# Kernel tuning notes

Measured on AMD Instinct MI355X. Metric: run time of the kernel, lower is better.

The kernel has to match this reference:

```python
import jax, jax.numpy as jnp
import numpy as np


def _conv1x1(x, w, b=None):
    # x: (N,C,H,W), w: (O,C) -> (N,O,H,W)
    y = jnp.einsum('nchw,oc->nohw', x, w)
    return y if b is None else y + b[None, :, None, None]


def _norm(f):
    # per-channel zero-mean / unit-std over (N,H,W); torch.std is unbiased (ddof=1)
    mean = f.mean(axis=(0, 2, 3), keepdims=True)
    std = f.std(axis=(0, 2, 3), ddof=1, keepdims=True)
    return (f - mean) / (std + 1e-6)


def _causal_attention(x, w_cls):
    N, C, H, W = x.shape
    M = _conv1x1(x, w_cls).reshape(N, -1, H * W)     # (N,K,HW)
    sm = jax.nn.softmax(M, axis=2)                   # softmax over spatial
    return jnp.einsum('nkp,ncp->nkc', sm, x.reshape(N, C, H * W))  # (N,K,C)


def _ccnet(x, wq, bq, wk, bk, wv, bv, gamma1):
    B, C, H, W = x.shape
    q = _conv1x1(x, wq, bq)  # (B,Cq,H,W)
    k = _conv1x1(x, wk, bk)
    v = _conv1x1(x, wv, bv)  # (B,C,H,W)
    # column (vertical) attention energies with -inf on the self diagonal
    eH = jnp.einsum('bciw,bcjw->biwj', q, k)         # (B,H,W,H)
    eH = jnp.where(jnp.eye(H, dtype=bool)[None, :, None, :], -jnp.inf, eH)
    # row (horizontal) attention energies
    eW = jnp.einsum('bchi,bchj->bhij', q, k)         # (B,H,W,W)
    att = jax.nn.softmax(jnp.concatenate([eH, eW], axis=3), axis=3)
    attH, attW = att[..., :H], att[..., H:]
    outH = jnp.einsum('bcjw,biwj->bciw', v, attH)    # aggregate along column
    outW = jnp.einsum('bchj,bhij->bchi', v, attW)    # aggregate along row
    return gamma1 * (outH + outW) + x


def setup_inputs() -> dict:
    key = jax.random.key(0)
    ks = jax.random.split(key, 10)
    B, C, H, W = 8, 256, 96, 96
    Cq, K = C // 8, 6
    f32 = jnp.float32
    return {
        'preds_S': jax.random.normal(ks[0], (B, C, H, W), f32),
        'preds_T': jax.random.normal(ks[1], (B, C, H, W), f32),
        'w_cls': jax.random.normal(ks[2], (K, C), f32) * 0.05,
        'wq': jax.random.normal(ks[3], (Cq, C), f32) * 0.05,
        'bq': jnp.zeros((Cq,), f32),
        'wk': jax.random.normal(ks[4], (Cq, C), f32) * 0.05,
        'bk': jnp.zeros((Cq,), f32),
        'wv': jax.random.normal(ks[5], (C, C), f32) * 0.05,
        'bv': jnp.zeros((C,), f32),
        'gamma1': jax.random.normal(ks[6], (1,), f32) * 0.1,
    }


def reference(preds_S, preds_T, w_cls, wq, bq, wk, bk, wv, bv, gamma1):
    CA_W, CC_W = 0.0005, 1e-05
    N = preds_S.shape[0]
    s = _norm(preds_S)
    t = _norm(preds_T)
    ca_t = _causal_attention(t, w_cls)
    ca_s = _causal_attention(s, w_cls)
    ca_loss = jnp.sum((ca_t - ca_s) ** 2) / N
    cc_t = _ccnet(t, wq, bq, wk, bk, wv, bv, gamma1)
    cc_s = _ccnet(s, wq, bq, wk, bk, wv, bv, gamma1)
    cc_loss = jnp.sum((cc_t - cc_s) ** 2) / N
    return ca_loss * CA_W + cc_loss * CC_W
```

## Files before the change

kernel.cpp:

```cpp
#include <hip/hip_runtime.h>
#include <math.h>

#define NBAT 8
#define NC   256
#define NH   96
#define NW   96
#define NP   9216
#define NCQ  32
#define NKC  6
#define NL   192
#define NV   320
#define NTOT 73728

typedef __attribute__((ext_vector_type(4))) float  floatx4;
typedef __attribute__((ext_vector_type(8))) short  short8;

__device__ __forceinline__ float bf2f(unsigned short h){
  return __uint_as_float(((unsigned)h) << 16);
}
__device__ __forceinline__ float bflo(unsigned u){ return __uint_as_float(u << 16); }
__device__ __forceinline__ float bfhi(unsigned u){ return __uint_as_float(u & 0xFFFF0000u); }
__device__ __forceinline__ unsigned short f2bf(float f){
  unsigned u = __float_as_uint(f);
  u += 0x7FFFu + ((u >> 16) & 1u);
  return (unsigned short)(u >> 16);
}

union F4 { float4 v; float a[4]; };

__device__ __forceinline__ float warpReduceSum(float v){
  #pragma unroll
  for (int m = 32; m; m >>= 1) v += __shfl_xor(v, m);
  return v;
}
__device__ __forceinline__ float warpReduceMax(float v){
  #pragma unroll
  for (int m = 32; m; m >>= 1) v = fmaxf(v, __shfl_xor(v, m));
  return v;
}
__device__ float blockReduceSum(float v){
  __shared__ float lds[8];
  v = warpReduceSum(v);
  int wid = threadIdx.x >> 6, lane = threadIdx.x & 63;
  int nw = blockDim.x >> 6;
  if (lane == 0) lds[wid] = v;
  __syncthreads();
  if (wid == 0){
    v = (lane < nw) ? lds[lane] : 0.f;
    #pragma unroll
    for (int m = 4; m; m >>= 1) v += __shfl_xor(v, m);
  }
  __syncthreads();
  return v;
}
__device__ float blockReduceMax(float v){
  __shared__ float lds[8];
  v = warpReduceMax(v);
  int wid = threadIdx.x >> 6, lane = threadIdx.x & 63;
  int nw = blockDim.x >> 6;
  if (lane == 0) lds[wid] = v;
  __syncthreads();
  if (wid == 0){
    v = (lane < nw) ? lds[lane] : -INFINITY;
    #pragma unroll
    for (int m = 4; m; m >>= 1) v = fmaxf(v, __shfl_xor(v, m));
  }
  __syncthreads();
  return v;
}

__global__ __launch_bounds__(256)
void k_stats(const float* __restrict__ S, const float* __restrict__ T,
             float* __restrict__ s_sum, float* __restrict__ s_sq){
  int blk = blockIdx.x;
  int t = blk / (NC * NBAT);
  int rem = blk % (NC * NBAT);
  int c = rem / NBAT;
  int n = rem % NBAT;
  const float4* x4 = (const float4*)((t ? T : S) + ((size_t)n * NC + c) * NP);
  float s = 0.f, q = 0.f;
  for (int p = threadIdx.x; p < NP / 4; p += 256){
    F4 f; f.v = x4[p];
    #pragma unroll
    for (int j = 0; j < 4; j++){ s += f.a[j]; q += f.a[j] * f.a[j]; }
  }
  s = blockReduceSum(s);
  q = blockReduceSum(q);
  if (threadIdx.x == 0){
    atomicAdd(&s_sum[t * NC + c], s);
    atomicAdd(&s_sq[t * NC + c], q);
  }
}

__global__ __launch_bounds__(512)
void k_finalize(const float* __restrict__ s_sum, const float* __restrict__ s_sq,
                float* __restrict__ mean, float* __restrict__ inv){
  int i = threadIdx.x;
  if (i < 2 * NC){
    float s = s_sum[i], q = s_sq[i];
    float m = s / (float)NTOT;
    float var = (q - s * m) / (float)(NTOT - 1);
    var = fmaxf(var, 0.f);
    mean[i] = m;
    inv[i] = 1.f / (sqrtf(var) + 1e-6f);
  }
}

__global__ __launch_bounds__(256)
void k_caM(const float* __restrict__ S, const float* __restrict__ T,
           const float* __restrict__ wcls,
           const float* __restrict__ mean, const float* __restrict__ inv,
           float* __restrict__ smca){
  int pt = blockIdx.x, n = blockIdx.y, t = blockIdx.z;
  __shared__ float wsc[NKC * NC];
  __shared__ float shift[NKC];
  for (int idx = threadIdx.x; idx < NKC * NC; idx += 256){
    int c = idx & 255;
    wsc[idx] = wcls[idx] * inv[t * NC + c];
  }
  __syncthreads();
  if (threadIdx.x < NKC){
    float sh = 0.f;
    for (int c = 0; c < NC; c++) sh += wsc[threadIdx.x * NC + c] * mean[t * NC + c];
    shift[threadIdx.x] = sh;
  }
  __syncthreads();
  int p = pt * 256 + threadIdx.x;
  const float* x = (t ? T : S) + (size_t)n * NC * NP + p;
  float acc[NKC];
  #pragma unroll
  for (int k = 0; k < NKC; k++) acc[k] = 0.f;
  for (int c = 0; c < NC; c++){
    float xv = x[(size_t)c * NP];
    #pragma unroll
    for (int k = 0; k < NKC; k++) acc[k] += wsc[k * NC + c] * xv;
  }
  size_t base = ((size_t)(t * NBAT + n) * NKC) * NP + p;
  #pragma unroll
  for (int k = 0; k < NKC; k++) smca[base + (size_t)k * NP] = acc[k] - shift[k];
}

__global__ __launch_bounds__(256)
void k_caSoftmax(float* __restrict__ smca){
  int r = blockIdx.x;
  float* row = smca + (size_t)r * NP;
  float m = -INFINITY;
  for (int p = threadIdx.x; p < NP; p += 256) m = fmaxf(m, row[p]);
  m = blockReduceMax(m);
  __shared__ float bm, bs;
  if (threadIdx.x == 0) bm = m;
  __syncthreads();
  m = bm;
  float s = 0.f;
  for (int p = threadIdx.x; p < NP; p += 256) s += expf(row[p] - m);
  s = blockReduceSum(s);
  if (threadIdx.x == 0) bs = 1.f / s;
  __syncthreads();
  float rs = bs;
  for (int p = threadIdx.x; p < NP; p += 256) row[p] = expf(row[p] - m) * rs;
}

__global__ __launch_bounds__(256)
void k_caOut(const float* __restrict__ S, const float* __restrict__ T,
             const float* __restrict__ smca,
             const float* __restrict__ mean, const float* __restrict__ inv,
             float* __restrict__ ca){
  int ct = blockIdx.x & 7, ks = blockIdx.x >> 3;
  int n = blockIdx.y, t = blockIdx.z;
  int c0 = ct * 32;
  __shared__ float xt[32 * 264];
  __shared__ float smt[NKC * 256];
  int cl = threadIdx.x >> 3, pl = threadIdx.x & 7;
  float acc[NKC];
  #pragma unroll
  for (int k = 0; k < NKC; k++) acc[k] = 0.f;
  const float* xbase = (t ? T : S) + (size_t)n * NC * NP;
  const float* smbase = smca + (size_t)(t * NBAT + n) * NKC * NP;
  for (int pt = ks * 6; pt < ks * 6 + 6; pt++){
    int p0 = pt * 256;
    for (int idx = threadIdx.x; idx < 32 * 256; idx += 256){
      int r = idx >> 8, p = idx & 255;
      float v = xbase[(size_t)(c0 + r) * NP + p0 + p];
      xt[r * 264 + p] = (v - mean[t * NC + c0 + r]) * inv[t * NC + c0 + r];
    }
    for (int idx = threadIdx.x; idx < NKC * 256; idx += 256){
      int k = idx >> 8, p = idx & 255;
      smt[idx] = smbase[(size_t)k * NP + p0 + p];
    }
    __syncthreads();
    for (int j = 0; j < 32; j++){
      float xv = xt[cl * 264 + pl + 8 * j];
      #pragma unroll
      for (int k = 0; k < NKC; k++) acc[k] += smt[k * 256 + pl + 8 * j] * xv;
    }
    __syncthreads();
  }
  #pragma unroll
  for (int k = 0; k < NKC; k++){
    float v = acc[k];
    v += __shfl_xor(v, 1); v += __shfl_xor(v, 2); v += __shfl_xor(v, 4);
    if (pl == 0) atomicAdd(&ca[((size_t)(t * NBAT + n) * NKC + k) * NC + c0 + cl], v);
  }
}

__global__ __launch_bounds__(256)
void k_caLoss(const float* __restrict__ ca, float* __restrict__ out){
  int i = blockIdx.x * 256 + threadIdx.x;
  float d = 0.f;
  if (i < NBAT * NKC * NC) d = ca[(size_t)NBAT * NKC * NC + i] - ca[i];
  float ss = blockReduceSum(d * d);
  if (threadIdx.x == 0) atomicAdd(out, ss * (0.0005f / 8.0f));
}

__global__ __launch_bounds__(256)
void k_xn(const float* __restrict__ x0, int b0,
          const float* __restrict__ mean, const float* __restrict__ inv, int t,
          unsigned short* __restrict__ XN){
  int pt = blockIdx.x, ct = blockIdx.y, bb = blockIdx.z;
  int bg = b0 + bb;
  int p0 = pt * 64, c0 = ct * 64;
  __shared__ float tile[64 * 65];
  const float* x = x0 + ((size_t)bg * NC + c0) * NP + p0;
  #pragma unroll
  for (int i = 0; i < 4; i++){
    int idx = threadIdx.x + i * 256;
    int r = idx >> 4, g = (idx & 15) * 4;
    F4 f; f.v = *(const float4*)(x + (size_t)r * NP + g);
    float m = mean[t * NC + c0 + r], iv = inv[t * NC + c0 + r];
    #pragma unroll
    for (int j = 0; j < 4; j++) tile[(g + j) * 65 + r] = (f.a[j] - m) * iv;
  }
  __syncthreads();
  #pragma unroll
  for (int i = 0; i < 4; i++){
    int idx = threadIdx.x + i * 256;
    int p = idx >> 4, g = (idx & 15) * 4;
    unsigned lo = (unsigned)f2bf(tile[p * 65 + g + 0]) | ((unsigned)f2bf(tile[p * 65 + g + 1]) << 16);
    unsigned hi = (unsigned)f2bf(tile[p * 65 + g + 2]) | ((unsigned)f2bf(tile[p * 65 + g + 3]) << 16);
    uint2 u; u.x = lo; u.y = hi;
    *(uint2*)(XN + ((size_t)bb * NP + p0 + p) * NC + c0 + g) = u;
  }
}

__global__ __launch_bounds__(256)
void k_wconv(const float* __restrict__ wv, const float* __restrict__ wq,
             const float* __restrict__ wk, unsigned short* __restrict__ Wb){
  int n = blockIdx.x;
  const float* src = (n < 256) ? (wv + (size_t)n * NC)
                   : (n < 288) ? (wq + (size_t)(n - 256) * NC)
                               : (wk + (size_t)(n - 288) * NC);
  Wb[(size_t)n * NC + threadIdx.x] = f2bf(src[threadIdx.x]);
}

__global__ __launch_bounds__(256)
void k_v(const unsigned short* __restrict__ XN, const unsigned short* __restrict__ Wb,
         const float* __restrict__ bv, const float* __restrict__ bq,
         const float* __restrict__ bk,
         unsigned short* __restrict__ VT1,
         unsigned short* __restrict__ qb, unsigned short* __restrict__ kb){
  int pt = blockIdx.x, bb = blockIdx.y;
  int p0 = pt * 64;
  __shared__ unsigned short Wl[NV * 40];
  int lane = threadIdx.x & 63;
  int wid = threadIdx.x >> 6;
  int col = lane & 15, quad = lane >> 4;
  const unsigned short* xnb = XN + (size_t)bb * NP * NC + (size_t)(p0 + wid * 16 + col) * NC;
  floatx4 acc[20];
  #pragma unroll
  for (int nt = 0; nt < 20; nt++) acc[nt] = (floatx4){0.f, 0.f, 0.f, 0.f};

  int ci_n[5], ci_k8[5];
  #pragma unroll
  for (int i = 0; i < 5; i++){ int ci = i * 256 + threadIdx.x; ci_n[i] = ci >> 2; ci_k8[i] = (ci & 3) * 8; }

  short8 w[5];
  #pragma unroll
  for (int i = 0; i < 5; i++)
    w[i] = *(const short8*)(Wb + (size_t)ci_n[i] * NC + ci_k8[i]);

  for (int ks = 0; ks < 8; ks++){
    if (ks) __syncthreads();
    #pragma unroll
    for (int i = 0; i < 5; i++)
      *(short8*)(Wl + ci_n[i] * 40 + ci_k8[i]) = w[i];
    __syncthreads();
    if (ks < 7){
      int k0n = (ks + 1) * 32;
      #pragma unroll
      for (int i = 0; i < 5; i++)
        w[i] = *(const short8*)(Wb + (size_t)ci_n[i] * NC + k0n + ci_k8[i]);
    }
    short8 a = *(const short8*)(xnb + ks * 32 + quad * 8);
    #pragma unroll
    for (int nt = 0; nt < 20; nt++){
      short8 b = *(const short8*)(Wl + (nt * 16 + col) * 40 + quad * 8);
      acc[nt] = __builtin_amdgcn_mfma_f32_16x16x32_bf16(a, b, acc[nt], 0, 0, 0);
    }
  }

  int prow0 = p0 + wid * 16 + quad * 4;
  #pragma unroll
  for (int nt = 0; nt < 16; nt++){
    int c = nt * 16 + col;
    float bias = bv[c];
    uint2 u;
    u.x = (unsigned)f2bf(acc[nt][0] + bias) | ((unsigned)f2bf(acc[nt][1] + bias) << 16);
    u.y = (unsigned)f2bf(acc[nt][2] + bias) | ((unsigned)f2bf(acc[nt][3] + bias) << 16);
    *(uint2*)(VT1 + ((size_t)bb * NC + c) * NP + prow0) = u;
  }
  #pragma unroll
  for (int nt = 16; nt < 18; nt++){
    int c = (nt - 16) * 16 + col;
    float bias = bq[c];
    #pragma unroll
    for (int i = 0; i < 4; i++)
      qb[((size_t)bb * NP + prow0 + i) * NCQ + c] = f2bf(acc[nt][i] + bias);
  }
  #pragma unroll
  for (int nt = 18; nt < 20; nt++){
    int c = (nt - 18) * 16 + col;
    float bias = bk[c];
    #pragma unroll
    for (int i = 0; i < 4; i++)
      kb[((size_t)bb * NP + prow0 + i) * NCQ + c] = f2bf(acc[nt][i] + bias);
  }
}

__global__ __launch_bounds__(256)
void k_vt(const unsigned short* __restrict__ VT1, unsigned short* __restrict__ VT2){
  int c = blockIdx.x, bb = blockIdx.y;
  __shared__ unsigned short tile[96 * 104];
  size_t base = ((size_t)bb * NC + c) * NP;
  for (int idx = threadIdx.x; idx < 1152; idx += 256){
    int h = idx / 12, g = idx % 12;
    short8 v = *(const short8*)(VT1 + base + h * 96 + g * 8);
    #pragma unroll
    for (int kk = 0; kk < 8; kk++) tile[(g * 8 + kk) * 104 + h] = ((unsigned short*)&v)[kk];
  }
  __syncthreads();
  for (int idx = threadIdx.x; idx < 1152; idx += 256){
    int w = idx / 12, g = idx % 12;
    short8 v = *(const short8*)(tile + w * 104 + g * 8);
    *(short8*)(VT2 + base + w * 96 + g * 8) = v;
  }
}

__global__ __launch_bounds__(256)
void k_e(const unsigned short* __restrict__ qb, const unsigned short* __restrict__ kb,
         unsigned short* __restrict__ att){
  int x = blockIdx.x, bb = blockIdx.y, which = blockIdx.z;
  int lane = threadIdx.x & 63, wid = threadIdx.x >> 6;
  int col = lane & 15, quad = lane >> 4;
  int mi0 = (wid & 1) * 3, ni0 = (wid >> 1) * 3;
  short8 a[3], b[3];
  if (which == 0){
    #pragma unroll
    for (int m = 0; m < 3; m++)
      a[m] = *(const short8*)(qb + ((size_t)bb * NP + ((mi0 + m) * 16 + col) * 96 + x) * NCQ + quad * 8);
    #pragma unroll
    for (int n = 0; n < 3; n++)
      b[n] = *(const short8*)(kb + ((size_t)bb * NP + ((ni0 + n) * 16 + col) * 96 + x) * NCQ + quad * 8);
  } else {
    #pragma unroll
    for (int m = 0; m < 3; m++)
      a[m] = *(const short8*)(qb + ((size_t)bb * NP + x * 96 + (mi0 + m) * 16 + col) * NCQ + quad * 8);
    #pragma unroll
    for (int n = 0; n < 3; n++)
      b[n] = *(const short8*)(kb + ((size_t)bb * NP + x * 96 + (ni0 + n) * 16 + col) * NCQ + quad * 8);
  }
  floatx4 acc[3][3];
  #pragma unroll
  for (int m = 0; m < 3; m++)
    #pragma unroll
    for (int n = 0; n < 3; n++){
      acc[m][n] = (floatx4){0.f, 0.f, 0.f, 0.f};
      acc[m][n] = __builtin_amdgcn_mfma_f32_16x16x32_bf16(a[m], b[n], acc[m][n], 0, 0, 0);
    }
  #pragma unroll
  for (int m = 0; m < 3; m++)
    #pragma unroll
    for (int n = 0; n < 3; n++){
      int j = (ni0 + n) * 16 + col;
      #pragma unroll
      for (int r = 0; r < 4; r++){
        int i = (mi0 + m) * 16 + quad * 4 + r;
        int p = which ? (x * 96 + i) : (i * 96 + x);
        float v = (!which && j == i) ? -INFINITY : acc[m][n][r];
        att[((size_t)bb * NP + p) * NL + (which ? 96 + j : j)] = f2bf(v);
      }
    }
}

__global__ __launch_bounds__(256)
void k_attSoftmax(unsigned short* __restrict__ att){
  int q = blockIdx.x * 4 + (threadIdx.x >> 6);
  int lane = threadIdx.x & 63;
  unsigned short* row = att + (size_t)q * NL;
  float e0 = bf2f(row[lane]);
  float e1 = bf2f(row[64 + lane]);
  float e2 = bf2f(row[128 + lane]);
  float m = fmaxf(e0, fmaxf(e1, e2));
  m = warpReduceMax(m);
  float x0 = expf(e0 - m), x1 = expf(e1 - m), x2 = expf(e2 - m);
  float s = warpReduceSum(x0 + x1 + x2);
  float rs = 1.f / s;
  row[lane]       = f2bf(x0 * rs);
  row[64 + lane]  = f2bf(x1 * rs);
  row[128 + lane] = f2bf(x2 * rs);
}

__global__ __launch_bounds__(256)
void k_outH(const unsigned short* __restrict__ VT2, const unsigned short* __restrict__ att,
            unsigned short* __restrict__ OH){
  int w = blockIdx.x, bb = blockIdx.y, cs = blockIdx.z;
  int lane = threadIdx.x & 63, wid = threadIdx.x >> 6;
  int col = lane & 15, quad = lane >> 4;
  int c = cs * 64 + wid * 16 + col;
  floatx4 acc[6];
  #pragma unroll
  for (int m = 0; m < 6; m++) acc[m] = (floatx4){0.f, 0.f, 0.f, 0.f};
  #pragma unroll
  for (int ks = 0; ks < 3; ks++){
    int k0 = ks * 32 + quad * 8;
    short8 a[6], b;
    #pragma unroll
    for (int m = 0; m < 6; m++)
      a[m] = *(const short8*)(att + ((size_t)bb * NP + (m * 16 + col) * 96 + w) * NL + k0);
    b = *(const short8*)(VT2 + ((size_t)bb * NC + c) * NP + w * 96 + k0);
    #pragma unroll
    for (int m = 0; m < 6; m++)
      acc[m] = __builtin_amdgcn_mfma_f32_16x16x32_bf16(a[m], b, acc[m], 0, 0, 0);
  }
  #pragma unroll
  for (int m = 0; m < 6; m++){
    #pragma unroll
    for (int r = 0; r < 4; r++){
      int i = m * 16 + quad * 4 + r;
      OH[((size_t)bb * NP + i * 96 + w) * NC + c] = f2bf(acc[m][r]);
    }
  }
}

__global__ __launch_bounds__(256)
void k_outW(const unsigned short* __restrict__ VT1, const unsigned short* __restrict__ att,
            const unsigned short* __restrict__ OH, unsigned short* __restrict__ Ot,
            const float* __restrict__ predsS, const float* __restrict__ predsT,
            const float* __restrict__ mean, const float* __restrict__ inv,
            const float* __restrict__ gamma, int b0, int spass,
            float* __restrict__ out){
  int h = blockIdx.x, bb = blockIdx.y, cs = blockIdx.z;
  int lane = threadIdx.x & 63, wid = threadIdx.x >> 6;
  int col = lane & 15, quad = lane >> 4;
  int c = cs * 64 + wid * 16 + col;
  floatx4 acc[6];
  #pragma unroll
  for (int m = 0; m < 6; m++) acc[m] = (floatx4){0.f, 0.f, 0.f, 0.f};
  #pragma unroll
  for (int ks = 0; ks < 3; ks++){
    int k0 = ks * 32 + quad * 8;
    short8 a[6], b;
    #pragma unroll
    for (int m = 0; m < 6; m++)
      a[m] = *(const short8*)(att + ((size_t)bb * NP + h * 96 + m * 16 + col) * NL + 96 + k0);
    b = *(const short8*)(VT1 + ((size_t)bb * NC + c) * NP + h * 96 + k0);
    #pragma unroll
    for (int m = 0; m < 6; m++)
      acc[m] = __builtin_amdgcn_mfma_f32_16x16x32_bf16(a[m], b, acc[m], 0, 0, 0);
  }
  if (!spass){
    #pragma unroll
    for (int m = 0; m < 6; m++){
      #pragma unroll
      for (int r = 0; r < 4; r++){
        int i = m * 16 + quad * 4 + r;
        size_t base = ((size_t)bb * NP + h * 96 + i) * NC + c;
        Ot[base] = f2bf(acc[m][r] + bf2f(OH[base]));
      }
    }
  } else {
    int bg = b0 + bb;
    float g = gamma[0];
    float ss = 0.f;
    float mS = mean[c],      iS = inv[c];
    float mT = mean[NC + c], iT = inv[NC + c];
    const float* tp = predsT + ((size_t)bg * NC + c) * NP + h * 96;
    const float* sp = predsS + ((size_t)bg * NC + c) * NP + h * 96;
    #pragma unroll
    for (int m = 0; m < 6; m++){
      int i0 = m * 16 + quad * 4;
      F4 tv, sv;
      tv.v = *(const float4*)(tp + i0);
      sv.v = *(const float4*)(sp + i0);
      #pragma unroll
      for (int r = 0; r < 4; r++){
        size_t base = ((size_t)bb * NP + h * 96 + i0 + r) * NC + c;
        float os = acc[m][r] + bf2f(OH[base]);
        float ot = bf2f(Ot[base]);
        float dn = (tv.a[r] - mT) * iT - (sv.a[r] - mS) * iS;
        float d = g * (ot - os) + dn;
        ss += d * d;
      }
    }
    ss = blockReduceSum(ss);
    if (threadIdx.x == 0) atomicAdd(out, ss * (1e-5f / 8.0f));
  }
}

extern "C" void kernel_launch(void* const* d_in, const int* in_sizes, int n_in,
                              void* d_out, int out_size, void* d_ws, size_t ws_size,
                              hipStream_t stream){
  (void)in_sizes; (void)n_in; (void)out_size;
  const float* S    = (const float*)d_in[0];
  const float* T    = (const float*)d_in[1];
  const float* wcls = (const float*)d_in[2];
  const float* wq   = (const float*)d_in[3];
  const float* bq   = (const float*)d_in[4];
  const float* wk   = (const float*)d_in[5];
  const float* bk   = (const float*)d_in[6];
  const float* wv   = (const float*)d_in[7];
  const float* bv   = (const float*)d_in[8];
  const float* gamma= (const float*)d_in[9];
  float* out = (float*)d_out;

  char* base = (char*)d_ws;
  size_t off = 0;
  auto alloc = [&](size_t b){ size_t o = off; off += (b + 255) & ~(size_t)255; return o; };
  size_t o_ssum = alloc(2 * NC * 4);
  size_t o_ssq  = alloc(2 * NC * 4);
  size_t o_mean = alloc(2 * NC * 4);
  size_t o_inv  = alloc(2 * NC * 4);
  size_t o_wb   = alloc((size_t)NV * NC * 2);
  size_t o_ca   = alloc((size_t)2 * NBAT * NKC * NC * 4);
  size_t o_smca = alloc((size_t)2 * NBAT * NKC * NP * 4);
  size_t fixed = off;
  size_t per_b = (size_t)NP * NC * 2 * 4
               + (size_t)NP * NCQ * 2 * 2
               + (size_t)NP * NL * 2;
  int NB = 8;
  while (NB > 1 && fixed + (size_t)NB * per_b + 8192 > ws_size) NB >>= 1;

  size_t o_xn  = alloc((size_t)NB * NP * NC * 2);
  size_t o_v1  = alloc((size_t)NB * NP * NC * 2);
  size_t o_v2  = alloc((size_t)NB * NP * NC * 2);
  size_t o_q   = alloc((size_t)NB * NP * NCQ * 2);
  size_t o_k   = alloc((size_t)NB * NP * NCQ * 2);
  size_t o_att = alloc((size_t)NB * NP * NL * 2);
  size_t o_ot  = alloc((size_t)NB * NP * NC * 2);
  size_t o_oh  = o_xn;

  float* ssum = (float*)(base + o_ssum);
  float* ssq  = (float*)(base + o_ssq);
  float* mean = (float*)(base + o_mean);
  float* inv  = (float*)(base + o_inv);
  float* ca   = (float*)(base + o_ca);
  float* smca = (float*)(base + o_smca);
  unsigned short* Wb  = (unsigned short*)(base + o_wb);
  unsigned short* XN  = (unsigned short*)(base + o_xn);
  unsigned short* VT1 = (unsigned short*)(base + o_v1);
  unsigned short* VT2 = (unsigned short*)(base + o_v2);
  unsigned short* qbp = (unsigned short*)(base + o_q);
  unsigned short* kbp = (unsigned short*)(base + o_k);
  unsigned short* att = (unsigned short*)(base + o_att);
  unsigned short* OH  = (unsigned short*)(base + o_oh);
  unsigned short* Ot  = (unsigned short*)(base + o_ot);

  hipMemsetAsync(d_out, 0, 4, stream);
  hipMemsetAsync(base + o_ssum, 0, 4096, stream);
  hipMemsetAsync(base + o_ca, 0, (size_t)2 * NBAT * NKC * NC * 4, stream);

  k_stats<<<dim3(2 * NC * NBAT), 256, 0, stream>>>(S, T, ssum, ssq);
  k_finalize<<<1, 512, 0, stream>>>(ssum, ssq, mean, inv);
  k_wconv<<<dim3(NV), 256, 0, stream>>>(wv, wq, wk, Wb);

  k_caM<<<dim3(36, NBAT, 2), 256, 0, stream>>>(S, T, wcls, mean, inv, smca);
  k_caSoftmax<<<dim3(2 * NBAT * NKC), 256, 0, stream>>>(smca);
  k_caOut<<<dim3(48, NBAT, 2), 256, 0, stream>>>(S, T, smca, mean, inv, ca);
  k_caLoss<<<dim3(48), 256, 0, stream>>>(ca, out);

  for (int b0 = 0; b0 < NBAT; b0 += NB){
    for (int pass = 0; pass < 2; pass++){
      int t = (pass == 0) ? 1 : 0;
      const float* x = t ? T : S;
      k_xn<<<dim3(144, 4, NB), 256, 0, stream>>>(x, b0, mean, inv, t, XN);
      k_v<<<dim3(144, NB), 256, 0, stream>>>(XN, Wb, bv, bq, bk, VT1, qbp, kbp);
      k_vt<<<dim3(NC, NB), 256, 0, stream>>>(VT1, VT2);
      k_e<<<dim3(96, NB, 2), 256, 0, stream>>>(qbp, kbp, att);
      k_attSoftmax<<<dim3(NB * 2304), 256, 0, stream>>>(att);
      k_outH<<<dim3(96, NB, 4), 256, 0, stream>>>(VT2, att, OH);
      k_outW<<<dim3(96, NB, 4), 256, 0, stream>>>(VT1, att, OH, Ot, S, T, mean, inv,
                                                  gamma, b0, pass, out);
    }
  }
}
```

Baseline: 689.2 us.

## Process teacher and student per batch together and fuse output-W with loss

The CCNet section now loops over one batch at a time and handles the teacher and student streams in the same launches, using a grid dimension to select between them. This replaces the earlier two passes over a multi-batch chunk. The new k_outWL kernel computes both outW results, stages both outH tiles in shared memory, and reduces the loss directly, so the intermediate Ot buffer is no longer written and read back. The smaller per-batch working set may stay resident in cache. In exchange there are many more, smaller kernel launches whose grids may not fill the GPU.

```diff
diff --git a/kernel.cpp b/kernel.cpp
--- a/kernel.cpp
+++ b/kernel.cpp
@@ -18,8 +18,6 @@
 __device__ __forceinline__ float bf2f(unsigned short h){
   return __uint_as_float(((unsigned)h) << 16);
 }
-__device__ __forceinline__ float bflo(unsigned u){ return __uint_as_float(u << 16); }
-__device__ __forceinline__ float bfhi(unsigned u){ return __uint_as_float(u & 0xFFFF0000u); }
 __device__ __forceinline__ unsigned short f2bf(float f){
   unsigned u = __float_as_uint(f);
   u += 0x7FFFu + ((u >> 16) & 1u);
@@ -213,11 +211,13 @@
 }
 
 __global__ __launch_bounds__(256)
-void k_xn(const float* __restrict__ x0, int b0,
-          const float* __restrict__ mean, const float* __restrict__ inv, int t,
-          unsigned short* __restrict__ XN){
-  int pt = blockIdx.x, ct = blockIdx.y, bb = blockIdx.z;
-  int bg = b0 + bb;
+void k_xn(const float* __restrict__ S, const float* __restrict__ T, int bg,
+          const float* __restrict__ mean, const float* __restrict__ inv,
+          unsigned short* __restrict__ XNT, unsigned short* __restrict__ XNS){
+  int pt = blockIdx.x, ct = blockIdx.y, ts = blockIdx.z;
+  int t = ts ? 0 : 1;
+  const float* x0 = ts ? S : T;
+  unsigned short* XN = ts ? XNS : XNT;
   int p0 = pt * 64, c0 = ct * 64;
   __shared__ float tile[64 * 65];
   const float* x = x0 + ((size_t)bg * NC + c0) * NP + p0;
@@ -238,7 +238,7 @@
     unsigned lo = (unsigned)f2bf(tile[p * 65 + g + 0]) | ((unsigned)f2bf(tile[p * 65 + g + 1]) << 16);
     unsigned hi = (unsigned)f2bf(tile[p * 65 + g + 2]) | ((unsigned)f2bf(tile[p * 65 + g + 3]) << 16);
     uint2 u; u.x = lo; u.y = hi;
-    *(uint2*)(XN + ((size_t)bb * NP + p0 + p) * NC + c0 + g) = u;
+    *(uint2*)(XN + ((size_t)(p0 + p)) * NC + c0 + g) = u;
   }
 }
 
@@ -253,18 +253,24 @@
 }
 
 __global__ __launch_bounds__(256)
-void k_v(const unsigned short* __restrict__ XN, const unsigned short* __restrict__ Wb,
+void k_v(const unsigned short* __restrict__ XNT, const unsigned short* __restrict__ XNS,
+         const unsigned short* __restrict__ Wb,
          const float* __restrict__ bv, const float* __restrict__ bq,
          const float* __restrict__ bk,
-         unsigned short* __restrict__ VT1,
-         unsigned short* __restrict__ qb, unsigned short* __restrict__ kb){
-  int pt = blockIdx.x, bb = blockIdx.y;
+         unsigned short* __restrict__ VT1T, unsigned short* __restrict__ VT1S,
+         unsigned short* __restrict__ qT, unsigned short* __restrict__ kT,
+         unsigned short* __restrict__ qS, unsigned short* __restrict__ kS){
+  int pt = blockIdx.x, ts = blockIdx.y;
+  const unsigned short* XN = ts ? XNS : XNT;
+  unsigned short* VT1 = ts ? VT1S : VT1T;
+  unsigned short* qb  = ts ? qS : qT;
+  unsigned short* kb  = ts ? kS : kT;
   int p0 = pt * 64;
   __shared__ unsigned short Wl[NV * 40];
   int lane = threadIdx.x & 63;
   int wid = threadIdx.x >> 6;
   int col = lane & 15, quad = lane >> 4;
-  const unsigned short* xnb = XN + (size_t)bb * NP * NC + (size_t)(p0 + wid * 16 + col) * NC;
+  const unsigned short* xnb = XN + (size_t)(p0 + wid * 16 + col) * NC;
   floatx4 acc[20];
   #pragma unroll
   for (int nt = 0; nt < 20; nt++) acc[nt] = (floatx4){0.f, 0.f, 0.f, 0.f};
@@ -306,7 +312,7 @@
     uint2 u;
     u.x = (unsigned)f2bf(acc[nt][0] + bias) | ((unsigned)f2bf(acc[nt][1] + bias) << 16);
     u.y = (unsigned)f2bf(acc[nt][2] + bias) | ((unsigned)f2bf(acc[nt][3] + bias) << 16);
-    *(uint2*)(VT1 + ((size_t)bb * NC + c) * NP + prow0) = u;
+    *(uint2*)(VT1 + (size_t)c * NP + prow0) = u;
   }
   #pragma unroll
   for (int nt = 16; nt < 18; nt++){
@@ -314,7 +320,7 @@
     float bias = bq[c];
     #pragma unroll
     for (int i = 0; i < 4; i++)
-      qb[((size_t)bb * NP + prow0 + i) * NCQ + c] = f2bf(acc[nt][i] + bias);
+      qb[((size_t)(prow0 + i)) * NCQ + c] = f2bf(acc[nt][i] + bias);
   }
   #pragma unroll
   for (int nt = 18; nt < 20; nt++){
@@ -322,15 +328,18 @@
     float bias = bk[c];
     #pragma unroll
     for (int i = 0; i < 4; i++)
-      kb[((size_t)bb * NP + prow0 + i) * NCQ + c] = f2bf(acc[nt][i] + bias);
-  }
-}
-
-__global__ __launch_bounds__(256)
-void k_vt(const unsigned short* __restrict__ VT1, unsigned short* __restrict__ VT2){
-  int c = blockIdx.x, bb = blockIdx.y;
+      kb[((size_t)(prow0 + i)) * NCQ + c] = f2bf(acc[nt][i] + bias);
+  }
+}
+
+__global__ __launch_bounds__(256)
+void k_vt(const unsigned short* __restrict__ VT1T, const unsigned short* __restrict__ VT1S,
+          unsigned short* __restrict__ VT2T, unsigned short* __restrict__ VT2S){
+  int c = blockIdx.x, ts = blockIdx.y;
+  const unsigned short* VT1 = ts ? VT1S : VT1T;
+  unsigned short* VT2 = ts ? VT2S : VT2T;
   __shared__ unsigned short tile[96 * 104];
-  size_t base = ((size_t)bb * NC + c) * NP;
+  size_t base = (size_t)c * NP;
   for (int idx = threadIdx.x; idx < 1152; idx += 256){
     int h = idx / 12, g = idx % 12;
     short8 v = *(const short8*)(VT1 + base + h * 96 + g * 8);
@@ -346,9 +355,13 @@
 }
 
 __global__ __launch_bounds__(256)
-void k_e(const unsigned short* __restrict__ qb, const unsigned short* __restrict__ kb,
-         unsigned short* __restrict__ att){
-  int x = blockIdx.x, bb = blockIdx.y, which = blockIdx.z;
+void k_e(const unsigned short* __restrict__ qT, const unsigned short* __restrict__ kT,
+         const unsigned short* __restrict__ qS, const unsigned short* __restrict__ kS,
+         unsigned short* __restrict__ attT, unsigned short* __restrict__ attS){
+  int x = blockIdx.x, ts = blockIdx.y, which = blockIdx.z;
+  const unsigned short* qb = ts ? qS : qT;
+  const unsigned short* kb = ts ? kS : kT;
+  unsigned short* att = ts ? attS : attT;
   int lane = threadIdx.x & 63, wid = threadIdx.x >> 6;
   int col = lane & 15, quad = lane >> 4;
   int mi0 = (wid & 1) * 3, ni0 = (wid >> 1) * 3;
@@ -356,17 +369,17 @@
   if (which == 0){
     #pragma unroll
     for (int m = 0; m < 3; m++)
-      a[m] = *(const short8*)(qb + ((size_t)bb * NP + ((mi0 + m) * 16 + col) * 96 + x) * NCQ + quad * 8);
+      a[m] = *(const short8*)(qb + ((size_t)(((mi0 + m) * 16 + col) * 96 + x)) * NCQ + quad * 8);
     #pragma unroll
     for (int n = 0; n < 3; n++)
-      b[n] = *(const short8*)(kb + ((size_t)bb * NP + ((ni0 + n) * 16 + col) * 96 + x) * NCQ + quad * 8);
+      b[n] = *(const short8*)(kb + ((size_t)(((ni0 + n) * 16 + col) * 96 + x)) * NCQ + quad * 8);
   } else {
     #pragma unroll
     for (int m = 0; m < 3; m++)
-      a[m] = *(const short8*)(qb + ((size_t)bb * NP + x * 96 + (mi0 + m) * 16 + col) * NCQ + quad * 8);
+      a[m] = *(const short8*)(qb + ((size_t)(x * 96 + (mi0 + m) * 16 + col)) * NCQ + quad * 8);
     #pragma unroll
     for (int n = 0; n < 3; n++)
-      b[n] = *(const short8*)(kb + ((size_t)bb * NP + x * 96 + (ni0 + n) * 16 + col) * NCQ + quad * 8);
+      b[n] = *(const short8*)(kb + ((size_t)(x * 96 + (ni0 + n) * 16 + col)) * NCQ + quad * 8);
   }
   floatx4 acc[3][3];
   #pragma unroll
@@ -386,16 +399,17 @@
         int i = (mi0 + m) * 16 + quad * 4 + r;
         int p = which ? (x * 96 + i) : (i * 96 + x);
         float v = (!which && j == i) ? -INFINITY : acc[m][n][r];
-        att[((size_t)bb * NP + p) * NL + (which ? 96 + j : j)] = f2bf(v);
+        att[(size_t)p * NL + (which ? 96 + j : j)] = f2bf(v);
       }
     }
 }
 
 __global__ __launch_bounds__(256)
-void k_attSoftmax(unsigned short* __restrict__ att){
+void k_attSoftmax(unsigned short* __restrict__ attT, unsigned short* __restrict__ attS){
   int q = blockIdx.x * 4 + (threadIdx.x >> 6);
   int lane = threadIdx.x & 63;
-  unsigned short* row = att + (size_t)q * NL;
+  unsigned short* row = (q < NP) ? (attT + (size_t)q * NL)
+                                 : (attS + (size_t)(q - NP) * NL);
   float e0 = bf2f(row[lane]);
   float e1 = bf2f(row[64 + lane]);
   float e2 = bf2f(row[128 + lane]);
@@ -410,9 +424,13 @@
 }
 
 __global__ __launch_bounds__(256)
-void k_outH(const unsigned short* __restrict__ VT2, const unsigned short* __restrict__ att,
-            unsigned short* __restrict__ OH){
-  int w = blockIdx.x, bb = blockIdx.y, cs = blockIdx.z;
+void k_outH(const unsigned short* __restrict__ VT2T, const unsigned short* __restrict__ VT2S,
+            const unsigned short* __restrict__ attT, const unsigned short* __restrict__ attS,
+            unsigned short* __restrict__ OHT, unsigned short* __restrict__ OHS){
+  int w = blockIdx.x, ts = blockIdx.y, cs = blockIdx.z;
+  const unsigned short* VT2 = ts ? VT2S : VT2T;
+  const unsigned short* att = ts ? attS : attT;
+  unsigned short* OH = ts ? OHS : OHT;
   int lane = threadIdx.x & 63, wid = threadIdx.x >> 6;
   int col = lane & 15, quad = lane >> 4;
   int c = cs * 64 + wid * 16 + col;
@@ -425,8 +443,8 @@
     short8 a[6], b;
     #pragma unroll
     for (int m = 0; m < 6; m++)
-      a[m] = *(const short8*)(att + ((size_t)bb * NP + (m * 16 + col) * 96 + w) * NL + k0);
-    b = *(const short8*)(VT2 + ((size_t)bb * NC + c) * NP + w * 96 + k0);
+      a[m] = *(const short8*)(att + ((size_t)((m * 16 + col) * 96 + w)) * NL + k0);
+    b = *(const short8*)(VT2 + (size_t)c * NP + w * 96 + k0);
     #pragma unroll
     for (int m = 0; m < 6; m++)
       acc[m] = __builtin_amdgcn_mfma_f32_16x16x32_bf16(a[m], b, acc[m], 0, 0, 0);
@@ -436,80 +454,100 @@
     #pragma unroll
     for (int r = 0; r < 4; r++){
       int i = m * 16 + quad * 4 + r;
-      OH[((size_t)bb * NP + i * 96 + w) * NC + c] = f2bf(acc[m][r]);
-    }
-  }
-}
-
-__global__ __launch_bounds__(256)
-void k_outW(const unsigned short* __restrict__ VT1, const unsigned short* __restrict__ att,
-            const unsigned short* __restrict__ OH, unsigned short* __restrict__ Ot,
-            const float* __restrict__ predsS, const float* __restrict__ predsT,
-            const float* __restrict__ mean, const float* __restrict__ inv,
-            const float* __restrict__ gamma, int b0, int spass,
-            float* __restrict__ out){
-  int h = blockIdx.x, bb = blockIdx.y, cs = blockIdx.z;
+      OH[((size_t)(i * 96 + w)) * NC + c] = f2bf(acc[m][r]);
+    }
+  }
+}
+
+__global__ __launch_bounds__(256)
+void k_outWL(const unsigned short* __restrict__ VT1T, const unsigned short* __restrict__ attT,
+             const unsigned short* __restrict__ OHT,
+             const unsigned short* __restrict__ VT1S, const unsigned short* __restrict__ attS,
+             const unsigned short* __restrict__ OHS,
+             const float* __restrict__ predsS, const float* __restrict__ predsT,
+             const float* __restrict__ mean, const float* __restrict__ inv,
+             const float* __restrict__ gamma, int bg,
+             float* __restrict__ out){
+  int h = blockIdx.x, cs = blockIdx.y;
   int lane = threadIdx.x & 63, wid = threadIdx.x >> 6;
   int col = lane & 15, quad = lane >> 4;
-  int c = cs * 64 + wid * 16 + col;
-  floatx4 acc[6];
-  #pragma unroll
-  for (int m = 0; m < 6; m++) acc[m] = (floatx4){0.f, 0.f, 0.f, 0.f};
+  int cl = wid * 16 + col;
+  int c  = cs * 64 + cl;
+
+  __shared__ unsigned short ohT[96 * 72];
+  __shared__ unsigned short ohS[96 * 72];
+
+  #pragma unroll
+  for (int k = 0; k < 3; k++){
+    int g = threadIdx.x + k * 256;
+    int i = g >> 3, cc = (g & 7) * 8;
+    size_t ga = ((size_t)(h * 96 + i)) * NC + cs * 64 + cc;
+    *(short8*)(ohT + i * 72 + cc) = *(const short8*)(OHT + ga);
+    *(short8*)(ohS + i * 72 + cc) = *(const short8*)(OHS + ga);
+  }
+  __syncthreads();
+
+  floatx4 accT[6], accS[6];
+  #pragma unroll
+  for (int m = 0; m < 6; m++){
+    accT[m] = (floatx4){0.f, 0.f, 0.f, 0.f};
+    accS[m] = (floatx4){0.f, 0.f, 0.f, 0.f};
+  }
   #pragma unroll
   for (int ks = 0; ks < 3; ks++){
     int k0 = ks * 32 + quad * 8;
     short8 a[6], b;
     #pragma unroll
     for (int m = 0; m < 6; m++)
-      a[m] = *(const short8*)(att + ((size_t)bb * NP + h * 96 + m * 16 + col) * NL + 96 + k0);
-    b = *(const short8*)(VT1 + ((size_t)bb * NC + c) * NP + h * 96 + k0);
+      a[m] = *(const short8*)(attT + ((size_t)(h * 96 + m * 16 + col)) * NL + 96 + k0);
+    b = *(const short8*)(VT1T + (size_t)c * NP + h * 96 + k0);
     #pragma unroll
     for (int m = 0; m < 6; m++)
-      acc[m] = __builtin_amdgcn_mfma_f32_16x16x32_bf16(a[m], b, acc[m], 0, 0, 0);
-  }
-  if (!spass){
-    #pragma unroll
-    for (int m = 0; m < 6; m++){
-      #pragma unroll
-      for (int r = 0; r < 4; r++){
-        int i = m * 16 + quad * 4 + r;
-        size_t base = ((size_t)bb * NP + h * 96 + i) * NC + c;
-        Ot[base] = f2bf(acc[m][r] + bf2f(OH[base]));
-      }
-    }
-  } else {
-    int bg = b0 + bb;
-    float g = gamma[0];
-    float ss = 0.f;
-    float mS = mean[c],      iS = inv[c];
-    float mT = mean[NC + c], iT = inv[NC + c];
-    const float* tp = predsT + ((size_t)bg * NC + c) * NP + h * 96;
-    const float* sp = predsS + ((size_t)bg * NC + c) * NP + h * 96;
-    #pragma unroll
-    for (int m = 0; m < 6; m++){
-      int i0 = m * 16 + quad * 4;
-      F4 tv, sv;
-      tv.v = *(const float4*)(tp + i0);
-      sv.v = *(const float4*)(sp + i0);
-      #pragma unroll
-      for (int r = 0; r < 4; r++){
-        size_t base = ((size_t)bb * NP + h * 96 + i0 + r) * NC + c;
-        float os = acc[m][r] + bf2f(OH[base]);
-        float ot = bf2f(Ot[base]);
-        float dn = (tv.a[r] - mT) * iT - (sv.a[r] - mS) * iS;
-        float d = g * (ot - os) + dn;
-        ss += d * d;
-      }
-    }
-    ss = blockReduceSum(ss);
-    if (threadIdx.x == 0) atomicAdd(out, ss * (1e-5f / 8.0f));
-  }
+      accT[m] = __builtin_amdgcn_mfma_f32_16x16x32_bf16(a[m], b, accT[m], 0, 0, 0);
+  }
+  #pragma unroll
+  for (int ks = 0; ks < 3; ks++){
+    int k0 = ks * 32 + quad * 8;
+    short8 a[6], b;
+    #pragma unroll
+    for (int m = 0; m < 6; m++)
+      a[m] = *(const short8*)(attS + ((size_t)(h * 96 + m * 16 + col)) * NL + 96 + k0);
+    b = *(const short8*)(VT1S + (size_t)c * NP + h * 96 + k0);
+    #pragma unroll
+    for (int m = 0; m < 6; m++)
+      accS[m] = __builtin_amdgcn_mfma_f32_16x16x32_bf16(a[m], b, accS[m], 0, 0, 0);
+  }
+
+  float g = gamma[0];
+  float ss = 0.f;
+  float mS = mean[c],      iS = inv[c];
+  float mT = mean[NC + c], iT = inv[NC + c];
+  const float* tp = predsT + ((size_t)bg * NC + c) * NP + h * 96;
+  const float* sp = predsS + ((size_t)bg * NC + c) * NP + h * 96;
+  #pragma unroll
+  for (int m = 0; m < 6; m++){
+    int i0 = m * 16 + quad * 4;
+    F4 tv, sv;
+    tv.v = *(const float4*)(tp + i0);
+    sv.v = *(const float4*)(sp + i0);
+    #pragma unroll
+    for (int r = 0; r < 4; r++){
+      int i = i0 + r;
+      float oT = accT[m][r] + bf2f(ohT[i * 72 + cl]);
+      float oS = accS[m][r] + bf2f(ohS[i * 72 + cl]);
+      float dn = (tv.a[r] - mT) * iT - (sv.a[r] - mS) * iS;
+      float d = g * (oT - oS) + dn;
+      ss += d * d;
+    }
+  }
+  ss = blockReduceSum(ss);
+  if (threadIdx.x == 0) atomicAdd(out, ss * (1e-5f / 8.0f));
 }
 
 extern "C" void kernel_launch(void* const* d_in, const int* in_sizes, int n_in,
                               void* d_out, int out_size, void* d_ws, size_t ws_size,
                               hipStream_t stream){
-  (void)in_sizes; (void)n_in; (void)out_size;
+  (void)in_sizes; (void)n_in; (void)out_size; (void)ws_size;
   const float* S    = (const float*)d_in[0];
   const float* T    = (const float*)d_in[1];
   const float* wcls = (const float*)d_in[2];
@@ -532,21 +570,22 @@
   size_t o_wb   = alloc((size_t)NV * NC * 2);
   size_t o_ca   = alloc((size_t)2 * NBAT * NKC * NC * 4);
   size_t o_smca = alloc((size_t)2 * NBAT * NKC * NP * 4);
-  size_t fixed = off;
-  size_t per_b = (size_t)NP * NC * 2 * 4
-               + (size_t)NP * NCQ * 2 * 2
-               + (size_t)NP * NL * 2;
-  int NB = 8;
-  while (NB > 1 && fixed + (size_t)NB * per_b + 8192 > ws_size) NB >>= 1;
-
-  size_t o_xn  = alloc((size_t)NB * NP * NC * 2);
-  size_t o_v1  = alloc((size_t)NB * NP * NC * 2);
-  size_t o_v2  = alloc((size_t)NB * NP * NC * 2);
-  size_t o_q   = alloc((size_t)NB * NP * NCQ * 2);
-  size_t o_k   = alloc((size_t)NB * NP * NCQ * 2);
-  size_t o_att = alloc((size_t)NB * NP * NL * 2);
-  size_t o_ot  = alloc((size_t)NB * NP * NC * 2);
-  size_t o_oh  = o_xn;
+
+  const size_t PB  = (size_t)NP * NC * 2;
+  const size_t ATT = (size_t)NP * NL * 2;
+  const size_t QB  = (size_t)NP * NCQ * 2;
+  size_t o_a  = alloc(PB);
+  size_t o_b  = alloc(PB);
+  size_t o_c  = alloc(PB);
+  size_t o_d  = alloc(PB);
+  size_t o_e  = alloc(PB);
+  size_t o_f  = alloc(PB);
+  size_t o_gT = alloc(ATT);
+  size_t o_gS = alloc(ATT);
+  size_t o_qT = alloc(QB);
+  size_t o_kT = alloc(QB);
+  size_t o_qS = alloc(QB);
+  size_t o_kS = alloc(QB);
 
   float* ssum = (float*)(base + o_ssum);
   float* ssq  = (float*)(base + o_ssq);
@@ -555,14 +594,18 @@
   float* ca   = (float*)(base + o_ca);
   float* smca = (float*)(base + o_smca);
   unsigned short* Wb  = (unsigned short*)(base + o_wb);
-  unsigned short* XN  = (unsigned short*)(base + o_xn);
-  unsigned short* VT1 = (unsigned short*)(base + o_v1);
-  unsigned short* VT2 = (unsigned short*)(base + o_v2);
-  unsigned short* qbp = (unsigned short*)(base + o_q);
-  unsigned short* kbp = (unsigned short*)(base + o_k);
-  unsigned short* att = (unsigned short*)(base + o_att);
-  unsigned short* OH  = (unsigned short*)(base + o_oh);
-  unsigned short* Ot  = (unsigned short*)(base + o_ot);
+  unsigned short* A   = (unsigned short*)(base + o_a);
+  unsigned short* B   = (unsigned short*)(base + o_b);
+  unsigned short* C   = (unsigned short*)(base + o_c);
+  unsigned short* D   = (unsigned short*)(base + o_d);
+  unsigned short* E   = (unsigned short*)(base + o_e);
+  unsigned short* F   = (unsigned short*)(base + o_f);
+  unsigned short* attT= (unsigned short*)(base + o_gT);
+  unsigned short* attS= (unsigned short*)(base + o_gS);
+  unsigned short* qT  = (unsigned short*)(base + o_qT);
+  unsigned short* kT  = (unsigned short*)(base + o_kT);
+  unsigned short* qS  = (unsigned short*)(base + o_qS);
+  unsigned short* kS  = (unsigned short*)(base + o_kS);
 
   hipMemsetAsync(d_out, 0, 4, stream);
   hipMemsetAsync(base + o_ssum, 0, 4096, stream);
@@ -577,18 +620,14 @@
   k_caOut<<<dim3(48, NBAT, 2), 256, 0, stream>>>(S, T, smca, mean, inv, ca);
   k_caLoss<<<dim3(48), 256, 0, stream>>>(ca, out);
 
-  for (int b0 = 0; b0 < NBAT; b0 += NB){
-    for (int pass = 0; pass < 2; pass++){
-      int t = (pass == 0) ? 1 : 0;
-      const float* x = t ? T : S;
-      k_xn<<<dim3(144, 4, NB), 256, 0, stream>>>(x, b0, mean, inv, t, XN);
-      k_v<<<dim3(144, NB), 256, 0, stream>>>(XN, Wb, bv, bq, bk, VT1, qbp, kbp);
-      k_vt<<<dim3(NC, NB), 256, 0, stream>>>(VT1, VT2);
-      k_e<<<dim3(96, NB, 2), 256, 0, stream>>>(qbp, kbp, att);
-      k_attSoftmax<<<dim3(NB * 2304), 256, 0, stream>>>(att);
-      k_outH<<<dim3(96, NB, 4), 256, 0, stream>>>(VT2, att, OH);
-      k_outW<<<dim3(96, NB, 4), 256, 0, stream>>>(VT1, att, OH, Ot, S, T, mean, inv,
-                                                  gamma, b0, pass, out);
-    }
-  }
-}
+  for (int bg = 0; bg < NBAT; bg++){
+    k_xn<<<dim3(144, 4, 2), 256, 0, stream>>>(S, T, bg, mean, inv, A, C);
+    k_v<<<dim3(144, 2), 256, 0, stream>>>(A, C, Wb, bv, bq, bk, B, D, qT, kT, qS, kS);
+    k_vt<<<dim3(256, 2), 256, 0, stream>>>(B, D, C , E );
+    k_e<<<dim3(96, 2, 2), 256, 0, stream>>>(qT, kT, qS, kS, attT, attS);
+    k_attSoftmax<<<dim3(2 * NP / 4), 256, 0, stream>>>(attT, attS);
+    k_outH<<<dim3(96, 2, 4), 256, 0, stream>>>(C, E, attT, attS, A , F );
+    k_outWL<<<dim3(96, 4), 256, 0, stream>>>(B, attT, A, D, attS, F, S, T, mean, inv,
+                                             gamma, bg, out);
+  }
+}
```

Result: slower. 859.2 us (+24.7%).
